# Kernel tuning notes

Hardware: AMD Instinct MI355X
Metric: run time of the kernel (lower is better)

Reference implementation:

```python
import jax, jax.numpy as jnp
import numpy as np
from jax import lax

EPS = 1e-5

def _pool_matrix(in_size, out_size):
    # adaptive avg pool: bin i covers [floor(i*in/out), ceil((i+1)*in/out))
    M = np.zeros((out_size, in_size), np.float32)
    for i in range(out_size):
        s = (i * in_size) // out_size
        e = -((-(i + 1) * in_size) // out_size)
        M[i, s:e] = 1.0 / (e - s)
    return jnp.asarray(M)

def _bn(x, w, b, m, v):
    # inference-mode BatchNorm2d, params shaped (C,)
    scale = w / jnp.sqrt(v + EPS)
    return x * scale[None, :, None, None] + (b - m * scale)[None, :, None, None]

def _conv3x3(x, w, b):
    y = lax.conv_general_dilated(x, w, (1, 1), 'SAME',
                                 dimension_numbers=('NCHW', 'OIHW', 'NCHW'))
    return y + b[None, :, None, None]

def setup_inputs() -> dict:
    key = jax.random.key(0)
    ks = iter(jax.random.split(key, 32))
    n = lambda shape, s=0.05: jax.random.normal(next(ks), shape, jnp.float32) * s
    d = {}
    d['master_grid'] = jax.random.normal(next(ks), (4096, 128, 16, 16), jnp.float32)
    # channel_reduce 1x1 conv (stored as (out,in)) + BN
    d['w_cr'] = n((32, 128), 0.1); d['b_cr'] = jnp.zeros((32,))
    d['bnr_w'] = jnp.ones((32,)); d['bnr_b'] = jnp.zeros((32,))
    d['bnr_m'] = n((32,), 0.1);   d['bnr_v'] = jnp.ones((32,))
    # self-attention 1x1 convs: q,k -> C//8=4 channels, v -> 32
    d['q_w'] = n((4, 32), 0.1);  d['q_b'] = jnp.zeros((4,))
    d['k_w'] = n((4, 32), 0.1);  d['k_b'] = jnp.zeros((4,))
    d['v_w'] = n((32, 32), 0.1); d['v_b'] = jnp.zeros((32,))
    d['gamma'] = jnp.full((1,), 0.15)
    # LayerNorm([32,7,8])
    d['ln_w'] = jnp.ones((32, 7, 8)); d['ln_b'] = jnp.zeros((32, 7, 8))
    # residual 3x3 conv + BN
    d['w_res'] = n((32, 32, 3, 3)); d['b_res'] = jnp.zeros((32,))
    d['bnres_w'] = jnp.ones((32,)); d['bnres_b'] = jnp.zeros((32,))
    d['bnres_m'] = n((32,), 0.1);   d['bnres_v'] = jnp.ones((32,))
    # conv1 3x3 -> 16 + BN
    d['w1'] = n((16, 32, 3, 3)); d['b1'] = jnp.zeros((16,))
    d['bn1_w'] = jnp.ones((16,)); d['bn1_b'] = jnp.zeros((16,))
    d['bn1_m'] = n((16,), 0.1);   d['bn1_v'] = jnp.ones((16,))
    # conv2 3x3 -> 1
    d['w2'] = n((1, 16, 3, 3)); d['b2'] = jnp.zeros((1,))
    return d

def reference(master_grid, w_cr, b_cr, bnr_w, bnr_b, bnr_m, bnr_v,
              q_w, q_b, k_w, k_b, v_w, v_b, gamma, ln_w, ln_b,
              w_res, b_res, bnres_w, bnres_b, bnres_m, bnres_v,
              w1, b1, bn1_w, bn1_b, bn1_m, bn1_v, w2, b2):
    B = master_grid.shape[0]
    Ph = _pool_matrix(16, 7)  # (7,16)
    Pw = _pool_matrix(16, 8)  # (8,16)
    # adaptive avg pool 16x16 -> 7x8
    x = jnp.einsum('bchw,ph,qw->bcpq', master_grid, Ph, Pw)  # (B,128,7,8)
    # 1x1 channel reduce + BN + ReLU
    x = jnp.einsum('bchw,oc->bohw', x, w_cr) + b_cr[None, :, None, None]
    x = jax.nn.relu(_bn(x, bnr_w, bnr_b, bnr_m, bnr_v))  # (B,32,7,8)
    # self-attention over 7*8=56 spatial positions
    q = (jnp.einsum('bchw,oc->bohw', x, q_w) + q_b[None, :, None, None]).reshape(B, 4, 56)
    k = (jnp.einsum('bchw,oc->bohw', x, k_w) + k_b[None, :, None, None]).reshape(B, 4, 56)
    v = (jnp.einsum('bchw,oc->bohw', x, v_w) + v_b[None, :, None, None]).reshape(B, 32, 56)
    attn = jax.nn.softmax(jnp.einsum('bdi,bdj->bij', q, k), axis=-1)  # (B,56,56)
    out = jnp.einsum('bcj,bij->bci', v, attn).reshape(B, 32, 7, 8)
    x = gamma * out + x
    # LayerNorm over (C,H,W)
    mu = jnp.mean(x, axis=(1, 2, 3), keepdims=True)
    var = jnp.var(x, axis=(1, 2, 3), keepdims=True)
    x = (x - mu) / jnp.sqrt(var + EPS) * ln_w[None] + ln_b[None]
    # residual conv block
    residual = x
    x = jax.nn.relu(_bn(_conv3x3(x, w_res, b_res), bnres_w, bnres_b, bnres_m, bnres_v))
    x = x + residual
    # head
    x = jax.nn.relu(_bn(_conv3x3(x, w1, b1), bn1_w, bn1_b, bn1_m, bn1_v))
    x = _conv3x3(x, w2, b2)  # (B,1,7,8)
    return x
```

## Files before the change

### kernel.cpp

```cpp
#include <hip/hip_runtime.h>
#include <hip/hip_bf16.h>

#define EPS 1e-5f

struct Params {
  const void* in[30];
  void* out;
};

template <bool BF>
__device__ __forceinline__ float ld(const void* p, int i) {
  if constexpr (BF) return __bfloat162float(((const __hip_bfloat16*)p)[i]);
  else return ((const float*)p)[i];
}

template <bool BF>
__device__ __forceinline__ float2 ld2(const void* p, int i) {
  if constexpr (BF) {
    __hip_bfloat162 v = *(const __hip_bfloat162*)(((const __hip_bfloat16*)p) + i);
    return make_float2(__bfloat162float(v.x), __bfloat162float(v.y));
  } else {
    return *(const float2*)(((const float*)p) + i);
  }
}

template <bool BF>
__device__ void body(const Params& P, int b, int t,
                     float* smem, float* s_x, float* red) {
  const int gbase = b * (128 * 256);

  const int hs[7] = {0, 2, 4, 6, 9, 11, 13};
  const int hl[7] = {3, 3, 3, 4, 3, 3, 3};
  float* xp = smem;
  for (int k = t; k < 128 * 56; k += 256) {
    int c = k / 56, r = k % 56, p = r >> 3, q = r & 7;
    int h0 = hs[p], n = hl[p];
    int base = gbase + c * 256 + h0 * 16 + 2 * q;
    float s = 0.f;
    for (int hh = 0; hh < n; ++hh) {
      float2 v2 = ld2<BF>(P.in[0], base + hh * 16);
      s += v2.x + v2.y;
    }
    xp[k] = s * (1.f / (float)(2 * n));
  }
  __syncthreads();

  for (int k = t; k < 32 * 56; k += 256) {
    int o = k / 56, s = k % 56;
    float acc = 0.f;
    for (int c = 0; c < 128; c += 2) {
      float2 w2 = ld2<BF>(P.in[1], o * 128 + c);
      acc = fmaf(w2.x, xp[c * 56 + s], acc);
      acc = fmaf(w2.y, xp[(c + 1) * 56 + s], acc);
    }
    acc += ld<BF>(P.in[2], o);
    float scale = ld<BF>(P.in[3], o) * rsqrtf(ld<BF>(P.in[6], o) + EPS);
    float z = acc * scale + (ld<BF>(P.in[4], o) - ld<BF>(P.in[5], o) * scale);
    s_x[k] = fmaxf(z, 0.f);
  }
  __syncthreads();

  float* aq = smem;
  float* ak = aq + 224;
  float* av = ak + 224;
  float* S = av + 1792;

  if (t < 224) {
    int d = t / 56, s = t % 56;
    float accq = 0.f, acck = 0.f;
    for (int o = 0; o < 32; ++o) {
      float xv = s_x[o * 56 + s];
      accq = fmaf(ld<BF>(P.in[7], d * 32 + o), xv, accq);
      acck = fmaf(ld<BF>(P.in[9], d * 32 + o), xv, acck);
    }
    aq[t] = accq + ld<BF>(P.in[8], d);
    ak[t] = acck + ld<BF>(P.in[10], d);
  }
  for (int k = t; k < 1792; k += 256) {
    int c = k / 56, s = k % 56;
    float acc = 0.f;
    for (int o = 0; o < 32; ++o)
      acc = fmaf(ld<BF>(P.in[11], c * 32 + o), s_x[o * 56 + s], acc);
    av[k] = acc + ld<BF>(P.in[12], c);
  }
  __syncthreads();

  for (int k = t; k < 3136; k += 256) {
    int i = k / 56, j = k % 56;
    float acc = 0.f;
    for (int d = 0; d < 4; ++d)
      acc = fmaf(aq[d * 56 + i], ak[d * 56 + j], acc);
    S[i * 57 + j] = acc;
  }
  __syncthreads();

  if (t < 56) {
    float* row = S + t * 57;
    float m = row[0];
    for (int j = 1; j < 56; ++j) m = fmaxf(m, row[j]);
    float sum = 0.f;
    for (int j = 0; j < 56; ++j) {
      float e = __expf(row[j] - m);
      row[j] = e;
      sum += e;
    }
    float inv = 1.f / sum;
    for (int j = 0; j < 56; ++j) row[j] *= inv;
  }
  __syncthreads();

  float gamma = ld<BF>(P.in[13], 0);
  float xr[7];
  for (int j7 = 0; j7 < 7; ++j7) {
    int k = t + j7 * 256;
    int c = k / 56, i = k % 56;
    float acc = 0.f;
    for (int j = 0; j < 56; ++j)
      acc = fmaf(av[c * 56 + j], S[i * 57 + j], acc);
    xr[j7] = gamma * acc + s_x[k];
  }

  float lsum = 0.f, lsq = 0.f;
  for (int j7 = 0; j7 < 7; ++j7) {
    lsum += xr[j7];
    lsq = fmaf(xr[j7], xr[j7], lsq);
  }
  for (int off = 32; off > 0; off >>= 1) {
    lsum += __shfl_down(lsum, off);
    lsq += __shfl_down(lsq, off);
  }
  __syncthreads();
  for (int k = t; k < 7200; k += 256) smem[k] = 0.f;
  if ((t & 63) == 0) {
    red[(t >> 6) * 2] = lsum;
    red[(t >> 6) * 2 + 1] = lsq;
  }
  __syncthreads();
  if (t == 0) {
    float sum = red[0] + red[2] + red[4] + red[6];
    float sq = red[1] + red[3] + red[5] + red[7];
    float mean = sum * (1.f / 1792.f);
    float var = sq * (1.f / 1792.f) - mean * mean;
    red[8] = mean;
    red[9] = rsqrtf(var + EPS);
  }
  __syncthreads();
  float mean = red[8], rstd = red[9];
  float* xln = smem;
  float* x2 = smem + 2880;
  float* h1 = smem + 5760;
  for (int j7 = 0; j7 < 7; ++j7) {
    int k = t + j7 * 256;
    int c = k / 56, s = k % 56, p = s >> 3, q = s & 7;
    float v = (xr[j7] - mean) * rstd * ld<BF>(P.in[14], k) + ld<BF>(P.in[15], k);
    xln[c * 90 + (p + 1) * 10 + (q + 1)] = v;
  }
  __syncthreads();

  if (t < 224) {
    int o = t & 31, p = t >> 5;
    float acc[8] = {0, 0, 0, 0, 0, 0, 0, 0};
    for (int ic = 0; ic < 32; ++ic) {
      for (int kh = 0; kh < 3; ++kh) {
        const float* row = xln + ic * 90 + (p + kh) * 10;
        float rv[10];
        for (int x = 0; x < 10; ++x) rv[x] = row[x];
        float w0 = ld<BF>(P.in[16], o * 288 + ic * 9 + kh * 3 + 0);
        float w1 = ld<BF>(P.in[16], o * 288 + ic * 9 + kh * 3 + 1);
        float w2 = ld<BF>(P.in[16], o * 288 + ic * 9 + kh * 3 + 2);
        for (int q = 0; q < 8; ++q)
          acc[q] = fmaf(rv[q], w0, fmaf(rv[q + 1], w1, fmaf(rv[q + 2], w2, acc[q])));
      }
    }
    float scale = ld<BF>(P.in[18], o) * rsqrtf(ld<BF>(P.in[21], o) + EPS);
    float bias = (ld<BF>(P.in[17], o) - ld<BF>(P.in[20], o)) * scale + ld<BF>(P.in[19], o);
    for (int q = 0; q < 8; ++q) {
      int idx = o * 90 + (p + 1) * 10 + (q + 1);
      x2[idx] = fmaxf(acc[q] * scale + bias, 0.f) + xln[idx];
    }
  }
  __syncthreads();

  if (t < 224) {
    int half = t / 112, rem = t % 112, o = rem & 15, p = rem >> 4;
    int q0 = half * 4;
    float acc[4] = {0, 0, 0, 0};
    for (int ic = 0; ic < 32; ++ic) {
      for (int kh = 0; kh < 3; ++kh) {
        const float* row = x2 + ic * 90 + (p + kh) * 10 + q0;
        float rv[6];
        for (int x = 0; x < 6; ++x) rv[x] = row[x];
        float w0 = ld<BF>(P.in[22], o * 288 + ic * 9 + kh * 3 + 0);
        float w1 = ld<BF>(P.in[22], o * 288 + ic * 9 + kh * 3 + 1);
        float w2 = ld<BF>(P.in[22], o * 288 + ic * 9 + kh * 3 + 2);
        for (int q = 0; q < 4; ++q)
          acc[q] = fmaf(rv[q], w0, fmaf(rv[q + 1], w1, fmaf(rv[q + 2], w2, acc[q])));
      }
    }
    float scale = ld<BF>(P.in[24], o) * rsqrtf(ld<BF>(P.in[27], o) + EPS);
    float bias = (ld<BF>(P.in[23], o) - ld<BF>(P.in[26], o)) * scale + ld<BF>(P.in[25], o);
    for (int q = 0; q < 4; ++q)
      h1[o * 90 + (p + 1) * 10 + (q0 + q + 1)] = fmaxf(acc[q] * scale + bias, 0.f);
  }
  __syncthreads();

  if (t < 56) {
    int p = t >> 3, q = t & 7;
    float acc = ld<BF>(P.in[29], 0);
    for (int ic = 0; ic < 16; ++ic) {
      for (int kh = 0; kh < 3; ++kh) {
        const float* row = h1 + ic * 90 + (p + kh) * 10 + q;
        acc = fmaf(row[0], ld<BF>(P.in[28], ic * 9 + kh * 3 + 0),
              fmaf(row[1], ld<BF>(P.in[28], ic * 9 + kh * 3 + 1),
              fmaf(row[2], ld<BF>(P.in[28], ic * 9 + kh * 3 + 2), acc)));
      }
    }
    if constexpr (BF)
      ((__hip_bfloat16*)P.out)[b * 56 + t] = __float2bfloat16(acc);
    else
      ((float*)P.out)[b * 56 + t] = acc;
  }
}

__launch_bounds__(256, 4)
__global__ void occ_decoder_kernel(Params P) {
  __shared__ __align__(16) float smem[7200];
  __shared__ __align__(16) float s_x[32 * 56];
  __shared__ float red[16];

  unsigned w0 = *(const unsigned*)P.in[3];
  bool isbf16 = (w0 & 0xFFFFu) != 0u;

  if (isbf16) body<true>(P, blockIdx.x, threadIdx.x, smem, s_x, red);
  else        body<false>(P, blockIdx.x, threadIdx.x, smem, s_x, red);
}

extern "C" void kernel_launch(void* const* d_in, const int* in_sizes, int n_in,
                              void* d_out, int out_size, void* d_ws, size_t ws_size,
                              hipStream_t stream) {
  Params P;
  for (int i = 0; i < 30; ++i) P.in[i] = d_in[i];
  P.out = d_out;
  int B = in_sizes[0] / (128 * 256);
  occ_decoder_kernel<<<dim3(B), dim3(256), 0, stream>>>(P);
}
```

Before: 1.346 ms.

## Shrink shared memory via chunked pooling, fp16 attention scores, and vectorized matmuls

Pools the input in two 64-channel halves and accumulates the channel-reduce projection across them, so the pooled buffer is half as large. Attention scores are stored as fp16 and softmax is spread over four lanes per row with shuffles. The channel-reduce, value projection and score loops now produce four outputs per thread using float4 shared-memory loads, and launch bounds rise to 6 blocks per SM. The goal is lower LDS use for higher occupancy plus fewer LDS instructions, at the cost of reduced precision in the attention weights and extra barriers.

```diff
diff --git a/kernel.cpp b/kernel.cpp
--- a/kernel.cpp
+++ b/kernel.cpp
@@ -1,5 +1,6 @@
 #include <hip/hip_runtime.h>
 #include <hip/hip_bf16.h>
+#include <hip/hip_fp16.h>
 
 #define EPS 1e-5f
 
@@ -25,45 +26,85 @@
 }
 
 template <bool BF>
-__device__ void body(const Params& P, int b, int t,
-                     float* smem, float* s_x, float* red) {
+__device__ __forceinline__ void acc_rows(const void* w, int wbase, const float* xp,
+                                         int g, float4& a) {
+  for (int c = 0; c < 64; c += 2) {
+    float2 w2 = ld2<BF>(w, wbase + c);
+    float4 xa = *(const float4*)(xp + c * 56 + 4 * g);
+    float4 xb = *(const float4*)(xp + (c + 1) * 56 + 4 * g);
+    a.x = fmaf(w2.x, xa.x, a.x); a.y = fmaf(w2.x, xa.y, a.y);
+    a.z = fmaf(w2.x, xa.z, a.z); a.w = fmaf(w2.x, xa.w, a.w);
+    a.x = fmaf(w2.y, xb.x, a.x); a.y = fmaf(w2.y, xb.y, a.y);
+    a.z = fmaf(w2.y, xb.z, a.z); a.w = fmaf(w2.y, xb.w, a.w);
+  }
+}
+
+template <bool BF>
+__device__ __forceinline__ float4 vproj(const void* w, int c, const float* s_x, int g) {
+  float4 a = {0.f, 0.f, 0.f, 0.f};
+  for (int o = 0; o < 32; ++o) {
+    float wv = ld<BF>(w, c * 32 + o);
+    float4 xv = *(const float4*)(s_x + o * 56 + 4 * g);
+    a.x = fmaf(wv, xv.x, a.x); a.y = fmaf(wv, xv.y, a.y);
+    a.z = fmaf(wv, xv.z, a.z); a.w = fmaf(wv, xv.w, a.w);
+  }
+  return a;
+}
+
+template <bool BF>
+__device__ void body(const Params& P, int b, int t, float* sm) {
   const int gbase = b * (128 * 256);
-
+  float* s_x = sm;
+  float* xp = sm + 1792;
   const int hs[7] = {0, 2, 4, 6, 9, 11, 13};
   const int hl[7] = {3, 3, 3, 4, 3, 3, 3};
-  float* xp = smem;
-  for (int k = t; k < 128 * 56; k += 256) {
-    int c = k / 56, r = k % 56, p = r >> 3, q = r & 7;
-    int h0 = hs[p], n = hl[p];
-    int base = gbase + c * 256 + h0 * 16 + 2 * q;
-    float s = 0.f;
-    for (int hh = 0; hh < n; ++hh) {
-      float2 v2 = ld2<BF>(P.in[0], base + hh * 16);
-      s += v2.x + v2.y;
-    }
-    xp[k] = s * (1.f / (float)(2 * n));
-  }
-  __syncthreads();
-
-  for (int k = t; k < 32 * 56; k += 256) {
-    int o = k / 56, s = k % 56;
-    float acc = 0.f;
-    for (int c = 0; c < 128; c += 2) {
-      float2 w2 = ld2<BF>(P.in[1], o * 128 + c);
-      acc = fmaf(w2.x, xp[c * 56 + s], acc);
-      acc = fmaf(w2.y, xp[(c + 1) * 56 + s], acc);
-    }
-    acc += ld<BF>(P.in[2], o);
-    float scale = ld<BF>(P.in[3], o) * rsqrtf(ld<BF>(P.in[6], o) + EPS);
-    float z = acc * scale + (ld<BF>(P.in[4], o) - ld<BF>(P.in[5], o) * scale);
-    s_x[k] = fmaxf(z, 0.f);
-  }
-  __syncthreads();
-
-  float* aq = smem;
-  float* ak = aq + 224;
-  float* av = ak + 224;
-  float* S = av + 1792;
+
+  const int m1 = 256 + t;
+  const int o0 = t / 14, g0 = t % 14;
+  const int o1 = m1 / 14, g1 = m1 % 14;
+  const bool has1 = (t < 192);
+
+  float4 acc0 = {0.f, 0.f, 0.f, 0.f};
+  float4 acc1 = {0.f, 0.f, 0.f, 0.f};
+  for (int r = 0; r < 2; ++r) {
+    for (int k = t; k < 64 * 56; k += 256) {
+      int c = k / 56, rr = k % 56, p = rr >> 3, q = rr & 7;
+      int h0 = hs[p], n = hl[p];
+      int base = gbase + (64 * r + c) * 256 + h0 * 16 + 2 * q;
+      float s = 0.f;
+      for (int hh = 0; hh < n; ++hh) {
+        float2 v2 = ld2<BF>(P.in[0], base + hh * 16);
+        s += v2.x + v2.y;
+      }
+      xp[k] = s * (1.f / (float)(2 * n));
+    }
+    __syncthreads();
+    acc_rows<BF>(P.in[1], o0 * 128 + 64 * r, xp, g0, acc0);
+    if (has1) acc_rows<BF>(P.in[1], o1 * 128 + 64 * r, xp, g1, acc1);
+    __syncthreads();
+  }
+  {
+    float sc = ld<BF>(P.in[3], o0) * rsqrtf(ld<BF>(P.in[6], o0) + EPS);
+    float sh = ld<BF>(P.in[4], o0) - ld<BF>(P.in[5], o0) * sc;
+    float bs = ld<BF>(P.in[2], o0);
+    *(float4*)(s_x + o0 * 56 + 4 * g0) =
+        make_float4(fmaxf((acc0.x + bs) * sc + sh, 0.f), fmaxf((acc0.y + bs) * sc + sh, 0.f),
+                    fmaxf((acc0.z + bs) * sc + sh, 0.f), fmaxf((acc0.w + bs) * sc + sh, 0.f));
+    if (has1) {
+      float sc1 = ld<BF>(P.in[3], o1) * rsqrtf(ld<BF>(P.in[6], o1) + EPS);
+      float sh1 = ld<BF>(P.in[4], o1) - ld<BF>(P.in[5], o1) * sc1;
+      float bs1 = ld<BF>(P.in[2], o1);
+      *(float4*)(s_x + o1 * 56 + 4 * g1) =
+          make_float4(fmaxf((acc1.x + bs1) * sc1 + sh1, 0.f), fmaxf((acc1.y + bs1) * sc1 + sh1, 0.f),
+                      fmaxf((acc1.z + bs1) * sc1 + sh1, 0.f), fmaxf((acc1.w + bs1) * sc1 + sh1, 0.f));
+    }
+  }
+  __syncthreads();
+
+  float* aq = sm + 1792;
+  float* ak = sm + 2016;
+  float* av = sm + 2240;
+  __half* Sb = (__half*)(sm + 4032);
 
   if (t < 224) {
     int d = t / 56, s = t % 56;
@@ -76,51 +117,89 @@
     aq[t] = accq + ld<BF>(P.in[8], d);
     ak[t] = acck + ld<BF>(P.in[10], d);
   }
-  for (int k = t; k < 1792; k += 256) {
-    int c = k / 56, s = k % 56;
-    float acc = 0.f;
-    for (int o = 0; o < 32; ++o)
-      acc = fmaf(ld<BF>(P.in[11], c * 32 + o), s_x[o * 56 + s], acc);
-    av[k] = acc + ld<BF>(P.in[12], c);
-  }
-  __syncthreads();
-
-  for (int k = t; k < 3136; k += 256) {
-    int i = k / 56, j = k % 56;
-    float acc = 0.f;
-    for (int d = 0; d < 4; ++d)
-      acc = fmaf(aq[d * 56 + i], ak[d * 56 + j], acc);
-    S[i * 57 + j] = acc;
-  }
-  __syncthreads();
-
-  if (t < 56) {
-    float* row = S + t * 57;
-    float m = row[0];
-    for (int j = 1; j < 56; ++j) m = fmaxf(m, row[j]);
-    float sum = 0.f;
-    for (int j = 0; j < 56; ++j) {
-      float e = __expf(row[j] - m);
-      row[j] = e;
-      sum += e;
-    }
-    float inv = 1.f / sum;
-    for (int j = 0; j < 56; ++j) row[j] *= inv;
+  {
+    float4 a = vproj<BF>(P.in[11], o0, s_x, g0);
+    float vb = ld<BF>(P.in[12], o0);
+    *(float4*)(av + o0 * 56 + 4 * g0) = make_float4(a.x + vb, a.y + vb, a.z + vb, a.w + vb);
+    if (has1) {
+      float4 a1 = vproj<BF>(P.in[11], o1, s_x, g1);
+      float vb1 = ld<BF>(P.in[12], o1);
+      *(float4*)(av + o1 * 56 + 4 * g1) = make_float4(a1.x + vb1, a1.y + vb1, a1.z + vb1, a1.w + vb1);
+    }
+  }
+  __syncthreads();
+
+  for (int it = 0; it < 4; ++it) {
+    int m = t + 256 * it;
+    if (m >= 784) break;
+    int i = m / 14, g = m % 14;
+    float4 a = {0.f, 0.f, 0.f, 0.f};
+#pragma unroll
+    for (int d = 0; d < 4; ++d) {
+      float qv = aq[d * 56 + i];
+      float4 kv = *(const float4*)(ak + d * 56 + 4 * g);
+      a.x = fmaf(qv, kv.x, a.x); a.y = fmaf(qv, kv.y, a.y);
+      a.z = fmaf(qv, kv.z, a.z); a.w = fmaf(qv, kv.w, a.w);
+    }
+    __half2* dst = (__half2*)(Sb + i * 58 + 4 * g);
+    dst[0] = __floats2half2_rn(a.x, a.y);
+    dst[1] = __floats2half2_rn(a.z, a.w);
+  }
+  __syncthreads();
+
+  if (t < 224) {
+    int i = t >> 2, z = t & 3;
+    __half* row = Sb + i * 58 + z * 14;
+    float v[14];
+    float mx = -3.0e38f;
+#pragma unroll
+    for (int j = 0; j < 7; ++j) {
+      float2 pr = __half22float2(*(const __half2*)(row + 2 * j));
+      v[2 * j] = pr.x;
+      v[2 * j + 1] = pr.y;
+      mx = fmaxf(mx, fmaxf(pr.x, pr.y));
+    }
+    mx = fmaxf(mx, __shfl_xor(mx, 1));
+    mx = fmaxf(mx, __shfl_xor(mx, 2));
+    float s = 0.f;
+#pragma unroll
+    for (int j = 0; j < 14; ++j) {
+      v[j] = __expf(v[j] - mx);
+      s += v[j];
+    }
+    s += __shfl_xor(s, 1);
+    s += __shfl_xor(s, 2);
+    float inv = 1.f / s;
+#pragma unroll
+    for (int j = 0; j < 7; ++j)
+      *(__half2*)(row + 2 * j) = __floats2half2_rn(v[2 * j] * inv, v[2 * j + 1] * inv);
   }
   __syncthreads();
 
   float gamma = ld<BF>(P.in[13], 0);
   float xr[7];
+#pragma unroll
   for (int j7 = 0; j7 < 7; ++j7) {
     int k = t + j7 * 256;
     int c = k / 56, i = k % 56;
-    float acc = 0.f;
-    for (int j = 0; j < 56; ++j)
-      acc = fmaf(av[c * 56 + j], S[i * 57 + j], acc);
-    xr[j7] = gamma * acc + s_x[k];
+    const __half* prow = Sb + i * 58;
+    const float* vrow = av + c * 56;
+    float a = 0.f;
+#pragma unroll
+    for (int j = 0; j < 56; j += 4) {
+      float4 vv = *(const float4*)(vrow + j);
+      float2 p0 = __half22float2(*(const __half2*)(prow + j));
+      float2 p1 = __half22float2(*(const __half2*)(prow + j + 2));
+      a = fmaf(vv.x, p0.x, a);
+      a = fmaf(vv.y, p0.y, a);
+      a = fmaf(vv.z, p1.x, a);
+      a = fmaf(vv.w, p1.y, a);
+    }
+    xr[j7] = gamma * a + s_x[k];
   }
 
   float lsum = 0.f, lsq = 0.f;
+#pragma unroll
   for (int j7 = 0; j7 < 7; ++j7) {
     lsum += xr[j7];
     lsq = fmaf(xr[j7], xr[j7], lsq);
@@ -130,7 +209,9 @@
     lsq += __shfl_down(lsq, off);
   }
   __syncthreads();
-  for (int k = t; k < 7200; k += 256) smem[k] = 0.f;
+  for (int k = t; k < 5760; k += 256) sm[k] = 0.f;
+  __syncthreads();
+  float* red = sm + 5750;
   if ((t & 63) == 0) {
     red[(t >> 6) * 2] = lsum;
     red[(t >> 6) * 2 + 1] = lsq;
@@ -146,9 +227,9 @@
   }
   __syncthreads();
   float mean = red[8], rstd = red[9];
-  float* xln = smem;
-  float* x2 = smem + 2880;
-  float* h1 = smem + 5760;
+  float* xln = sm;
+  float* x2 = sm + 2880;
+#pragma unroll
   for (int j7 = 0; j7 < 7; ++j7) {
     int k = t + j7 * 256;
     int c = k / 56, s = k % 56, p = s >> 3, q = s & 7;
@@ -161,44 +242,59 @@
     int o = t & 31, p = t >> 5;
     float acc[8] = {0, 0, 0, 0, 0, 0, 0, 0};
     for (int ic = 0; ic < 32; ++ic) {
+#pragma unroll
       for (int kh = 0; kh < 3; ++kh) {
-        const float* row = xln + ic * 90 + (p + kh) * 10;
-        float rv[10];
-        for (int x = 0; x < 10; ++x) rv[x] = row[x];
-        float w0 = ld<BF>(P.in[16], o * 288 + ic * 9 + kh * 3 + 0);
-        float w1 = ld<BF>(P.in[16], o * 288 + ic * 9 + kh * 3 + 1);
-        float w2 = ld<BF>(P.in[16], o * 288 + ic * 9 + kh * 3 + 2);
+        const float2* r2 = (const float2*)(xln + ic * 90 + (p + kh) * 10);
+        float2 a0 = r2[0], a1 = r2[1], a2 = r2[2], a3 = r2[3], a4 = r2[4];
+        float rv[10] = {a0.x, a0.y, a1.x, a1.y, a2.x, a2.y, a3.x, a3.y, a4.x, a4.y};
+        int wb = o * 288 + ic * 9 + kh * 3;
+        float w0 = ld<BF>(P.in[16], wb);
+        float w1 = ld<BF>(P.in[16], wb + 1);
+        float w2 = ld<BF>(P.in[16], wb + 2);
+#pragma unroll
         for (int q = 0; q < 8; ++q)
           acc[q] = fmaf(rv[q], w0, fmaf(rv[q + 1], w1, fmaf(rv[q + 2], w2, acc[q])));
       }
     }
     float scale = ld<BF>(P.in[18], o) * rsqrtf(ld<BF>(P.in[21], o) + EPS);
     float bias = (ld<BF>(P.in[17], o) - ld<BF>(P.in[20], o)) * scale + ld<BF>(P.in[19], o);
+#pragma unroll
     for (int q = 0; q < 8; ++q) {
       int idx = o * 90 + (p + 1) * 10 + (q + 1);
       x2[idx] = fmaxf(acc[q] * scale + bias, 0.f) + xln[idx];
     }
-  }
-  __syncthreads();
-
+  } else if (t - 224 < 10) {
+    sm[5750 + (t - 224)] = 0.f;
+  }
+  __syncthreads();
+
+  float* h1 = sm;
+  for (int k = t; k < 1440; k += 256) {
+    int rr = k % 90, col = rr % 10;
+    if (rr < 10 || rr >= 80 || col == 0 || col == 9) h1[k] = 0.f;
+  }
   if (t < 224) {
     int half = t / 112, rem = t % 112, o = rem & 15, p = rem >> 4;
     int q0 = half * 4;
     float acc[4] = {0, 0, 0, 0};
     for (int ic = 0; ic < 32; ++ic) {
+#pragma unroll
       for (int kh = 0; kh < 3; ++kh) {
-        const float* row = x2 + ic * 90 + (p + kh) * 10 + q0;
-        float rv[6];
-        for (int x = 0; x < 6; ++x) rv[x] = row[x];
-        float w0 = ld<BF>(P.in[22], o * 288 + ic * 9 + kh * 3 + 0);
-        float w1 = ld<BF>(P.in[22], o * 288 + ic * 9 + kh * 3 + 1);
-        float w2 = ld<BF>(P.in[22], o * 288 + ic * 9 + kh * 3 + 2);
+        const float2* r2 = (const float2*)(x2 + ic * 90 + (p + kh) * 10 + q0);
+        float2 a0 = r2[0], a1 = r2[1], a2 = r2[2];
+        float rv[6] = {a0.x, a0.y, a1.x, a1.y, a2.x, a2.y};
+        int wb = o * 288 + ic * 9 + kh * 3;
+        float w0 = ld<BF>(P.in[22], wb);
+        float w1 = ld<BF>(P.in[22], wb + 1);
+        float w2 = ld<BF>(P.in[22], wb + 2);
+#pragma unroll
         for (int q = 0; q < 4; ++q)
           acc[q] = fmaf(rv[q], w0, fmaf(rv[q + 1], w1, fmaf(rv[q + 2], w2, acc[q])));
       }
     }
     float scale = ld<BF>(P.in[24], o) * rsqrtf(ld<BF>(P.in[27], o) + EPS);
     float bias = (ld<BF>(P.in[23], o) - ld<BF>(P.in[26], o)) * scale + ld<BF>(P.in[25], o);
+#pragma unroll
     for (int q = 0; q < 4; ++q)
       h1[o * 90 + (p + 1) * 10 + (q0 + q + 1)] = fmaxf(acc[q] * scale + bias, 0.f);
   }
@@ -208,6 +304,7 @@
     int p = t >> 3, q = t & 7;
     float acc = ld<BF>(P.in[29], 0);
     for (int ic = 0; ic < 16; ++ic) {
+#pragma unroll
       for (int kh = 0; kh < 3; ++kh) {
         const float* row = h1 + ic * 90 + (p + kh) * 10 + q;
         acc = fmaf(row[0], ld<BF>(P.in[28], ic * 9 + kh * 3 + 0),
@@ -222,17 +319,15 @@
   }
 }
 
-__launch_bounds__(256, 4)
+__launch_bounds__(256, 6)
 __global__ void occ_decoder_kernel(Params P) {
-  __shared__ __align__(16) float smem[7200];
-  __shared__ __align__(16) float s_x[32 * 56];
-  __shared__ float red[16];
+  __shared__ __align__(16) float sm[5760];
 
   unsigned w0 = *(const unsigned*)P.in[3];
   bool isbf16 = (w0 & 0xFFFFu) != 0u;
 
-  if (isbf16) body<true>(P, blockIdx.x, threadIdx.x, smem, s_x, red);
-  else        body<false>(P, blockIdx.x, threadIdx.x, smem, s_x, red);
+  if (isbf16) body<true>(P, blockIdx.x, threadIdx.x, sm);
+  else        body<false>(P, blockIdx.x, threadIdx.x, sm);
 }
 
 extern "C" void kernel_launch(void* const* d_in, const int* in_sizes, int n_in,
```

After: 2.102 ms. +56.2%, slower.

## Shrink shared memory with fp16 intermediates and aliased buffers for occupancy

Applied to the files above, without the earlier changes.

Stores the pooled input and the attention score matrix in fp16 in shared memory. The pooled tile is transposed to a spatial-major layout so the channel-reduce loop can read half2 pairs, and the attention-times-V loop uses float2/half2 vector loads. All buffers are aliased into one 5776-float shared array, down from roughly 9000 floats, so more blocks can be resident per CU and fewer LDS instructions are issued. The cost is lost precision in the pooled activations and the softmax probabilities, which could push results past tolerance.

```diff
diff --git a/kernel.cpp b/kernel.cpp
--- a/kernel.cpp
+++ b/kernel.cpp
@@ -1,5 +1,6 @@
 #include <hip/hip_runtime.h>
 #include <hip/hip_bf16.h>
+#include <hip/hip_fp16.h>
 
 #define EPS 1e-5f
 
@@ -25,33 +26,34 @@
 }
 
 template <bool BF>
-__device__ void body(const Params& P, int b, int t,
-                     float* smem, float* s_x, float* red) {
+__device__ void body(const Params& P, int b, int t, float* sm) {
   const int gbase = b * (128 * 256);
-
-  const int hs[7] = {0, 2, 4, 6, 9, 11, 13};
-  const int hl[7] = {3, 3, 3, 4, 3, 3, 3};
-  float* xp = smem;
+  float* s_x = sm;
+  __half* xph = (__half*)(sm + 1792);
+
   for (int k = t; k < 128 * 56; k += 256) {
-    int c = k / 56, r = k % 56, p = r >> 3, q = r & 7;
-    int h0 = hs[p], n = hl[p];
+    int c = k / 56, rr = k % 56, p = rr >> 3, q = rr & 7;
+    int h0 = 2 * p + (p >= 4 ? 1 : 0);
+    int n = 3 + (p == 3 ? 1 : 0);
     int base = gbase + c * 256 + h0 * 16 + 2 * q;
-    float s = 0.f;
+    float sum = 0.f;
     for (int hh = 0; hh < n; ++hh) {
       float2 v2 = ld2<BF>(P.in[0], base + hh * 16);
-      s += v2.x + v2.y;
-    }
-    xp[k] = s * (1.f / (float)(2 * n));
+      sum += v2.x + v2.y;
+    }
+    xph[rr * 130 + c] = __float2half(sum * (n == 3 ? (1.f / 6.f) : 0.125f));
   }
   __syncthreads();
 
   for (int k = t; k < 32 * 56; k += 256) {
-    int o = k / 56, s = k % 56;
+    int o = k / 56, sp = k % 56;
+    const __half2* xrow = (const __half2*)xph + sp * 65;
     float acc = 0.f;
-    for (int c = 0; c < 128; c += 2) {
-      float2 w2 = ld2<BF>(P.in[1], o * 128 + c);
-      acc = fmaf(w2.x, xp[c * 56 + s], acc);
-      acc = fmaf(w2.y, xp[(c + 1) * 56 + s], acc);
+    for (int c2 = 0; c2 < 64; ++c2) {
+      float2 w2 = ld2<BF>(P.in[1], o * 128 + 2 * c2);
+      float2 xv = __half22float2(xrow[c2]);
+      acc = fmaf(w2.x, xv.x, acc);
+      acc = fmaf(w2.y, xv.y, acc);
     }
     acc += ld<BF>(P.in[2], o);
     float scale = ld<BF>(P.in[3], o) * rsqrtf(ld<BF>(P.in[6], o) + EPS);
@@ -60,16 +62,16 @@
   }
   __syncthreads();
 
-  float* aq = smem;
-  float* ak = aq + 224;
-  float* av = ak + 224;
-  float* S = av + 1792;
+  float* aq = sm + 1792;
+  float* ak = sm + 2016;
+  float* av = sm + 2240;
+  __half* Sb = (__half*)(sm + 4032);
 
   if (t < 224) {
-    int d = t / 56, s = t % 56;
+    int d = t / 56, sp = t % 56;
     float accq = 0.f, acck = 0.f;
     for (int o = 0; o < 32; ++o) {
-      float xv = s_x[o * 56 + s];
+      float xv = s_x[o * 56 + sp];
       accq = fmaf(ld<BF>(P.in[7], d * 32 + o), xv, accq);
       acck = fmaf(ld<BF>(P.in[9], d * 32 + o), xv, acck);
     }
@@ -77,10 +79,10 @@
     ak[t] = acck + ld<BF>(P.in[10], d);
   }
   for (int k = t; k < 1792; k += 256) {
-    int c = k / 56, s = k % 56;
+    int c = k / 56, sp = k % 56;
     float acc = 0.f;
     for (int o = 0; o < 32; ++o)
-      acc = fmaf(ld<BF>(P.in[11], c * 32 + o), s_x[o * 56 + s], acc);
+      acc = fmaf(ld<BF>(P.in[11], c * 32 + o), s_x[o * 56 + sp], acc);
     av[k] = acc + ld<BF>(P.in[12], c);
   }
   __syncthreads();
@@ -90,47 +92,67 @@
     float acc = 0.f;
     for (int d = 0; d < 4; ++d)
       acc = fmaf(aq[d * 56 + i], ak[d * 56 + j], acc);
-    S[i * 57 + j] = acc;
+    Sb[i * 58 + j] = __float2half(acc);
   }
   __syncthreads();
 
   if (t < 56) {
-    float* row = S + t * 57;
-    float m = row[0];
-    for (int j = 1; j < 56; ++j) m = fmaxf(m, row[j]);
+    __half* row = Sb + t * 58;
+    float m = __half2float(row[0]);
+    for (int j = 1; j < 56; ++j) m = fmaxf(m, __half2float(row[j]));
     float sum = 0.f;
     for (int j = 0; j < 56; ++j) {
-      float e = __expf(row[j] - m);
-      row[j] = e;
+      float e = __expf(__half2float(row[j]) - m);
+      row[j] = __float2half(e);
       sum += e;
     }
     float inv = 1.f / sum;
-    for (int j = 0; j < 56; ++j) row[j] *= inv;
+    for (int j = 0; j < 56; ++j)
+      row[j] = __float2half(__half2float(row[j]) * inv);
   }
   __syncthreads();
 
   float gamma = ld<BF>(P.in[13], 0);
-  float xr[7];
-  for (int j7 = 0; j7 < 7; ++j7) {
-    int k = t + j7 * 256;
-    int c = k / 56, i = k % 56;
-    float acc = 0.f;
-    for (int j = 0; j < 56; ++j)
-      acc = fmaf(av[c * 56 + j], S[i * 57 + j], acc);
-    xr[j7] = gamma * acc + s_x[k];
-  }
-
-  float lsum = 0.f, lsq = 0.f;
-  for (int j7 = 0; j7 < 7; ++j7) {
-    lsum += xr[j7];
-    lsq = fmaf(xr[j7], xr[j7], lsq);
-  }
+  float xr0, xr1, xr2, xr3, xr4, xr5, xr6;
+#define PHASE6(J, XR)                                          \
+  {                                                            \
+    int k = t + (J) * 256;                                     \
+    int c = k / 56, i = k % 56;                                \
+    const float2* vrow = (const float2*)(av + c * 56);         \
+    const __half2* prow = (const __half2*)(Sb + i * 58);       \
+    float a = 0.f;                                             \
+    for (int jj = 0; jj < 28; ++jj) {                          \
+      float2 vv = vrow[jj];                                    \
+      float2 pp = __half22float2(prow[jj]);                    \
+      a = fmaf(vv.x, pp.x, a);                                 \
+      a = fmaf(vv.y, pp.y, a);                                 \
+    }                                                          \
+    XR = fmaf(gamma, a, s_x[k]);                               \
+  }
+  PHASE6(0, xr0)
+  PHASE6(1, xr1)
+  PHASE6(2, xr2)
+  PHASE6(3, xr3)
+  PHASE6(4, xr4)
+  PHASE6(5, xr5)
+  PHASE6(6, xr6)
+#undef PHASE6
+
+  float lsum = xr0 + xr1 + xr2 + xr3 + xr4 + xr5 + xr6;
+  float lsq = xr0 * xr0;
+  lsq = fmaf(xr1, xr1, lsq);
+  lsq = fmaf(xr2, xr2, lsq);
+  lsq = fmaf(xr3, xr3, lsq);
+  lsq = fmaf(xr4, xr4, lsq);
+  lsq = fmaf(xr5, xr5, lsq);
+  lsq = fmaf(xr6, xr6, lsq);
   for (int off = 32; off > 0; off >>= 1) {
     lsum += __shfl_down(lsum, off);
     lsq += __shfl_down(lsq, off);
   }
   __syncthreads();
-  for (int k = t; k < 7200; k += 256) smem[k] = 0.f;
+  for (int k = t; k < 5760; k += 256) sm[k] = 0.f;
+  float* red = sm + 5760;
   if ((t & 63) == 0) {
     red[(t >> 6) * 2] = lsum;
     red[(t >> 6) * 2 + 1] = lsq;
@@ -146,15 +168,23 @@
   }
   __syncthreads();
   float mean = red[8], rstd = red[9];
-  float* xln = smem;
-  float* x2 = smem + 2880;
-  float* h1 = smem + 5760;
-  for (int j7 = 0; j7 < 7; ++j7) {
-    int k = t + j7 * 256;
-    int c = k / 56, s = k % 56, p = s >> 3, q = s & 7;
-    float v = (xr[j7] - mean) * rstd * ld<BF>(P.in[14], k) + ld<BF>(P.in[15], k);
-    xln[c * 90 + (p + 1) * 10 + (q + 1)] = v;
-  }
+  float* xln = sm;
+  float* x2 = sm + 2880;
+#define PHASE7(J, XR)                                                        \
+  {                                                                          \
+    int k = t + (J) * 256;                                                   \
+    int c = k / 56, sp = k % 56, p = sp >> 3, q = sp & 7;                    \
+    float v = (XR - mean) * rstd * ld<BF>(P.in[14], k) + ld<BF>(P.in[15], k);\
+    xln[c * 90 + (p + 1) * 10 + (q + 1)] = v;                                \
+  }
+  PHASE7(0, xr0)
+  PHASE7(1, xr1)
+  PHASE7(2, xr2)
+  PHASE7(3, xr3)
+  PHASE7(4, xr4)
+  PHASE7(5, xr5)
+  PHASE7(6, xr6)
+#undef PHASE7
   __syncthreads();
 
   if (t < 224) {
@@ -181,6 +211,7 @@
   }
   __syncthreads();
 
+  float* h1 = sm;
   if (t < 224) {
     int half = t / 112, rem = t % 112, o = rem & 15, p = rem >> 4;
     int q0 = half * 4;
@@ -224,15 +255,13 @@
 
 __launch_bounds__(256, 4)
 __global__ void occ_decoder_kernel(Params P) {
-  __shared__ __align__(16) float smem[7200];
-  __shared__ __align__(16) float s_x[32 * 56];
-  __shared__ float red[16];
+  __shared__ __align__(16) float sm[5776];
 
   unsigned w0 = *(const unsigned*)P.in[3];
   bool isbf16 = (w0 & 0xFFFFu) != 0u;
 
-  if (isbf16) body<true>(P, blockIdx.x, threadIdx.x, smem, s_x, red);
-  else        body<false>(P, blockIdx.x, threadIdx.x, smem, s_x, red);
+  if (isbf16) body<true>(P, blockIdx.x, threadIdx.x, sm);
+  else        body<false>(P, blockIdx.x, threadIdx.x, sm);
 }
 
 extern "C" void kernel_launch(void* const* d_in, const int* in_sizes, int n_in,
```

Measured after the change: 1.241 ms. -7.8%, faster.
